# Optimization experiments

Measured on AMD Instinct MI355X. Metric: run time of the kernel, lower is better.

## Reference

```python
import jax, jax.numpy as jnp
import numpy as np

B, S, D, H = 2, 2048, 1024, 16
HD = D // H  # head dim = 64


def setup_inputs() -> dict:
    key = jax.random.key(0)
    ks = jax.random.split(key, 9)
    std = 0.02
    return {
        "hidden_states": jax.random.normal(ks[0], (B, S, D), jnp.float32),
        "wq": jax.random.normal(ks[1], (D, D), jnp.float32) * std,
        "bq": jnp.zeros((D,), jnp.float32),
        "wk": jax.random.normal(ks[2], (D, D), jnp.float32) * std,
        "bk": jnp.zeros((D,), jnp.float32),
        "wv": jax.random.normal(ks[3], (D, D), jnp.float32) * std,
        "bv": jnp.zeros((D,), jnp.float32),
        "wo": jax.random.normal(ks[4], (D, D), jnp.float32) * std,
        "bo": jnp.zeros((D,), jnp.float32),
    }


def reference(hidden_states, wq, bq, wk, bk, wv, bv, wo, bo):
    b, s, d = hidden_states.shape
    # projections (torch Linear: x @ W.T + b; here weights stored as [in,out]-equivalent transpose)
    q = hidden_states @ wq.T + bq
    k = hidden_states @ wk.T + bk
    v = hidden_states @ wv.T + bv
    # [b, h, s, hd]
    q = q.reshape(b, s, H, HD).transpose(0, 2, 1, 3)
    k = k.reshape(b, s, H, HD).transpose(0, 2, 1, 3)
    v = v.reshape(b, s, H, HD).transpose(0, 2, 1, 3)
    scores = jnp.einsum("bhqd,bhkd->bhqk", q, k) / jnp.sqrt(jnp.float32(HD))
    probs = jax.nn.softmax(scores, axis=-1)  # dropout p=0 (eval)
    ctx = jnp.einsum("bhqk,bhkd->bhqd", probs, v)
    ctx = ctx.transpose(0, 2, 1, 3).reshape(b, s, d)
    return ctx @ wo.T + bo
```

## Files before the change

kernel.cpp:

```cpp
#include <hip/hip_runtime.h>
#include <math.h>
#include <stdint.h>

constexpr int BB  = 2;
constexpr int SS  = 2048;
constexpr int DD  = 1024;
constexpr int HH  = 16;
constexpr int HDD = 64;
constexpr int MM  = BB * SS;

typedef uint16_t u16;
typedef __attribute__((ext_vector_type(4))) float    f32x4;
typedef __attribute__((ext_vector_type(8))) _Float16 f16x8;
typedef __attribute__((ext_vector_type(4))) _Float16 f16x4;
typedef __attribute__((ext_vector_type(8))) short    s16x8;
typedef __attribute__((ext_vector_type(4))) unsigned int u32x4;

__device__ __forceinline__ u16 to_f16(float f) {
    const _Float16 h = (_Float16)f;
    return __builtin_bit_cast(u16, h);
}

__device__ __forceinline__ f32x4 mfma32(s16x8 a, s16x8 b, f32x4 c) {
    return __builtin_amdgcn_mfma_f32_16x16x32_f16(
        __builtin_bit_cast(f16x8, a), __builtin_bit_cast(f16x8, b), c, 0, 0, 0);
}
__device__ __forceinline__ f32x4 mfma32_ff(s16x8 a, f16x8 b, f32x4 c) {
    return __builtin_amdgcn_mfma_f32_16x16x32_f16(
        __builtin_bit_cast(f16x8, a), b, c, 0, 0, 0);
}

__device__ __forceinline__ void load_lds16(const void* g, void* l) {
    __builtin_amdgcn_global_load_lds(
        (const __attribute__((address_space(1))) void*)g,
        (__attribute__((address_space(3))) void*)l, 16, 0, 0);
}

__global__ __launch_bounds__(256) void cast_all(
    const float* __restrict__ x,
    const float* __restrict__ w0, const float* __restrict__ w1,
    const float* __restrict__ w2, const float* __restrict__ w3,
    u16* __restrict__ xb, u16* __restrict__ wb)
{
    const int blk = blockIdx.x, tid = threadIdx.x;
    const float* src; u16* dst; int idx;
    if (blk < 2048) { src = x; dst = xb; idx = blk * 256 + tid; }
    else {
        const int b2 = blk - 2048, which = b2 >> 9;
        src = (which == 0) ? w0 : (which == 1) ? w1 : (which == 2) ? w2 : w3;
        dst = wb + ((size_t)which << 20);
        idx = (b2 & 511) * 256 + tid;
    }
    const float4* in4 = (const float4*)src;
    const float4 a = in4[idx * 2], b = in4[idx * 2 + 1];
    s16x8 v;
    v[0] = (short)to_f16(a.x); v[1] = (short)to_f16(a.y);
    v[2] = (short)to_f16(a.z); v[3] = (short)to_f16(a.w);
    v[4] = (short)to_f16(b.x); v[5] = (short)to_f16(b.y);
    v[6] = (short)to_f16(b.z); v[7] = (short)to_f16(b.w);
    *(s16x8*)(dst + (size_t)idx * 8) = v;
}

template <bool SWAP>
__device__ __forceinline__ void kloop(
    const u16* __restrict__ Ag, const u16* __restrict__ Wg,
    u16* Abase, u16* Bbase, const int K, const int KH,
    const int c0, const int c1,
    const int lane, const int wm, const int wn, f32x4 (&acc)[4][4])
{
    load_lds16(Ag + (size_t)c0 * 16 * K, Abase + c0 * 512);
    load_lds16(Ag + (size_t)c1 * 16 * K, Abase + c1 * 512);
    load_lds16(Wg + (size_t)c0 * 16 * K, Bbase + c0 * 512);
    load_lds16(Wg + (size_t)c1 * 16 * K, Bbase + c1 * 512);

    for (int k0 = 0; k0 < KH; k0 += 32) {
        const int buf = (k0 >> 5) & 1;
        __syncthreads();
        if (k0 + 32 < KH) {
            const int nb_ = (buf ^ 1) * 4096;
            load_lds16(Ag + (size_t)c0 * 16 * K + k0 + 32, Abase + nb_ + c0 * 512);
            load_lds16(Ag + (size_t)c1 * 16 * K + k0 + 32, Abase + nb_ + c1 * 512);
            load_lds16(Wg + (size_t)c0 * 16 * K + k0 + 32, Bbase + nb_ + c0 * 512);
            load_lds16(Wg + (size_t)c1 * 16 * K + k0 + 32, Bbase + nb_ + c1 * 512);
        }
        const u16* Acur = Abase + buf * 4096;
        const u16* Bcur = Bbase + buf * 4096;

        s16x8 af[4], bf4[4];
#pragma unroll
        for (int i = 0; i < 4; ++i) {
            const int row = wm + i * 16 + (lane & 15);
            const int u   = (lane >> 4) ^ (row & 3);
            af[i] = *(const s16x8*)(Acur + (size_t)row * 32 + u * 8);
        }
#pragma unroll
        for (int j = 0; j < 4; ++j) {
            const int row = wn + j * 16 + (lane & 15);
            const int u   = (lane >> 4) ^ (row & 3);
            bf4[j] = *(const s16x8*)(Bcur + (size_t)row * 32 + u * 8);
        }
#pragma unroll
        for (int i = 0; i < 4; ++i)
#pragma unroll
            for (int j = 0; j < 4; ++j)
                acc[i][j] = SWAP ? mfma32(bf4[j], af[i], acc[i][j])
                                 : mfma32(af[i], bf4[j], acc[i][j]);
    }
}

template <int MODE>
__global__ __launch_bounds__(512) void gemm_mfma(
    const u16* __restrict__ A, const u16* __restrict__ Wb,
    const float* __restrict__ b0, const float* __restrict__ b1,
    const float* __restrict__ b2,
    float* __restrict__ outf, u16* __restrict__ outq, u16* __restrict__ outv,
    const int K)
{
    __shared__ u16 smem[32768];
    u16* As = smem;
    u16* Bs = smem + 16384;

    const int tid = threadIdx.x, lane = tid & 63, wid = tid >> 6;
    const int grp = wid >> 2, w4 = wid & 3;
    const int quad = lane >> 4;
    const int bm = blockIdx.y * 128;
    const int nb = blockIdx.x * 128;
    const int which = nb >> 10;
    const int ncol  = nb & 1023;
    const int KH = K >> 1;
    const u16* Wblk = Wb + ((size_t)which << 20) + (size_t)ncol * K;

    const int srow = lane >> 2;
    const int lu   = (lane & 3) ^ (srow & 3);
    const u16* Ag = A    + (size_t)(bm + srow) * K + grp * KH + lu * 8;
    const u16* Wg = Wblk + (size_t)srow       * K + grp * KH + lu * 8;
    const int c0 = w4 * 2, c1 = c0 + 1;
    u16* Abase = As + grp * 8192;
    u16* Bbase = Bs + grp * 8192;

    f32x4 acc[4][4];
#pragma unroll
    for (int i = 0; i < 4; ++i)
#pragma unroll
        for (int j = 0; j < 4; ++j) { f32x4 z = {0.f, 0.f, 0.f, 0.f}; acc[i][j] = z; }

    const int wm = (w4 >> 1) * 64, wn = (w4 & 1) * 64;
    const bool swap = (MODE == 0) || (which < 2);
    if (swap) kloop<true>(Ag, Wg, Abase, Bbase, K, KH, c0, c1, lane, wm, wn, acc);
    else      kloop<false>(Ag, Wg, Abase, Bbase, K, KH, c0, c1, lane, wm, wn, acc);

    __syncthreads();
    float* rp = (float*)smem;
    const int slot = (w4 * 64 + lane) * 4;
    if (grp == 1) {
#pragma unroll
        for (int i = 0; i < 4; ++i)
#pragma unroll
            for (int j = 0; j < 4; ++j)
                *(f32x4*)(rp + (i * 4 + j) * 1024 + slot) = acc[i][j];
    }
    __syncthreads();
    if (grp != 0) return;
#pragma unroll
    for (int i = 0; i < 4; ++i)
#pragma unroll
        for (int j = 0; j < 4; ++j)
            acc[i][j] += *(const f32x4*)(rp + (i * 4 + j) * 1024 + slot);

    if (MODE == 0) {
#pragma unroll
        for (int j = 0; j < 4; ++j) {
            const int n0 = nb + wn + 16 * j + quad * 4;
            const float4 bv = *(const float4*)&b0[n0];
#pragma unroll
            for (int i = 0; i < 4; ++i) {
                const int m = bm + wm + 16 * i + (lane & 15);
                f32x4 w = acc[i][j];
                w[0] += bv.x; w[1] += bv.y; w[2] += bv.z; w[3] += bv.w;
                *(f32x4*)&outf[(size_t)m * 1024 + n0] = w;
            }
        }
    } else if (which < 2) {
        const float* bias = which ? b1 : b0;
        const float scale = which ? 1.0f : 0.125f;
        u16* outb = outq + ((size_t)which << 22);
        const int h = (ncol + wn) >> 6;
#pragma unroll
        for (int j = 0; j < 4; ++j) {
            const int nl0 = ncol + wn + 16 * j + quad * 4;
            const float4 bv = *(const float4*)&bias[nl0];
            const int hd0 = 16 * j + quad * 4;
#pragma unroll
            for (int i = 0; i < 4; ++i) {
                const int m = bm + wm + 16 * i + (lane & 15);
                const int b_ = m >> 11, s = m & 2047;
                f16x4 w;
                w[0] = (_Float16)((acc[i][j][0] + bv.x) * scale);
                w[1] = (_Float16)((acc[i][j][1] + bv.y) * scale);
                w[2] = (_Float16)((acc[i][j][2] + bv.z) * scale);
                w[3] = (_Float16)((acc[i][j][3] + bv.w) * scale);
                *(f16x4*)&outb[(((size_t)(b_ * HH + h)) * SS + s) * HDD + hd0] = w;
            }
        }
    } else {
        const int kt = ((bm + wm) & 2047) >> 6;
        const int b_ = (bm + wm) >> 11;
#pragma unroll
        for (int j = 0; j < 4; ++j) {
            const int nl = ncol + wn + 16 * j + (lane & 15);
            const float bb = b2[nl];
            const int h = nl >> 6, hd = nl & 63;
            u16* vrow = outv + (((size_t)(b_ * HH + h)) * HDD + hd) * SS + kt * 64;
#pragma unroll
            for (int i = 0; i < 4; ++i) {
                const int p0 = (i >> 1) * 32 + quad * 8 + (i & 1) * 4;
                f16x4 w;
                w[0] = (_Float16)(acc[i][j][0] + bb);
                w[1] = (_Float16)(acc[i][j][1] + bb);
                w[2] = (_Float16)(acc[i][j][2] + bb);
                w[3] = (_Float16)(acc[i][j][3] + bb);
                *(f16x4*)&vrow[p0] = w;
            }
        }
    }
}

__global__ __launch_bounds__(512, 4) void attn_mfma(
    const u16* __restrict__ Q, const u16* __restrict__ Kg,
    const u16* __restrict__ Vt, u16* __restrict__ ctx)
{
    __shared__ u16 smem[32768];

    const int tid = threadIdx.x, lane = tid & 63, wid = tid >> 6;
    const int grp = wid >> 2, w4 = wid & 3;
    const int quad = lane >> 4;
    const int bh = blockIdx.y, q0 = blockIdx.x * 128;
    const u16* Qb = Q  + (size_t)bh * SS * HDD;
    const u16* Kb = Kg + (size_t)bh * SS * HDD + (size_t)grp * 1024 * HDD;
    const u16* Vb = Vt + (size_t)bh * HDD * SS + grp * 1024;

    u16* Kbase = smem + grp * 8192;
    u16* Vbase = smem + 16384 + grp * 8192;

    const int qa = q0 + w4 * 32 + (lane & 15);
    const s16x8 bq0a = *(const s16x8*)(Qb + (size_t)qa * HDD + quad * 8);
    const s16x8 bq1a = *(const s16x8*)(Qb + (size_t)qa * HDD + 32 + quad * 8);
    const s16x8 bq0b = *(const s16x8*)(Qb + (size_t)(qa + 16) * HDD + quad * 8);
    const s16x8 bq1b = *(const s16x8*)(Qb + (size_t)(qa + 16) * HDD + 32 + quad * 8);

    f32x4 oa[4], ob[4];
    f32x4 la4 = {0.f, 0.f, 0.f, 0.f}, lb4 = {0.f, 0.f, 0.f, 0.f};
#pragma unroll
    for (int m = 0; m < 4; ++m) {
        f32x4 z = {0.f, 0.f, 0.f, 0.f};
        oa[m] = z; ob[m] = z;
    }
    const s16x8 ones = {15360, 15360, 15360, 15360,
                        15360, 15360, 15360, 15360};

    const int c0 = w4 * 2, c1 = c0 + 1;
    const int r0 = (c0 * 64 + lane) >> 3, lu0 = ((lane & 7) ^ (r0 & 7));
    const int r1 = (c1 * 64 + lane) >> 3, lu1 = ((lane & 7) ^ (r1 & 7));
    const u16* Kp0 = Kb + (size_t)r0 * HDD + lu0 * 8;
    const u16* Kp1 = Kb + (size_t)r1 * HDD + lu1 * 8;
    const u16* Vp0 = Vb + (size_t)r0 * SS + lu0 * 8;
    const u16* Vp1 = Vb + (size_t)r1 * SS + lu1 * 8;

    load_lds16(Kp0, Kbase + c0 * 512);
    load_lds16(Kp1, Kbase + c1 * 512);
    load_lds16(Vp0, Vbase + c0 * 512);
    load_lds16(Vp1, Vbase + c1 * 512);

    for (int kt = 0; kt < 16; ++kt) {
        const int buf = kt & 1;
        __syncthreads();

        if (kt + 1 < 16) {
            const int nb_ = (buf ^ 1) * 4096;
            load_lds16(Kp0 + (size_t)(kt + 1) * 64 * HDD, Kbase + nb_ + c0 * 512);
            load_lds16(Kp1 + (size_t)(kt + 1) * 64 * HDD, Kbase + nb_ + c1 * 512);
            load_lds16(Vp0 + (kt + 1) * 64, Vbase + nb_ + c0 * 512);
            load_lds16(Vp1 + (kt + 1) * 64, Vbase + nb_ + c1 * 512);
        }
        const u16* Kbuf = Kbase + buf * 4096;
        const u16* Vbuf = Vbase + buf * 4096;

        f32x4 Sa[4], Sb[4];
#pragma unroll
        for (int j = 0; j < 4; ++j) {
            const int row = j * 16 + (lane & 15);
            const int sw = lane & 7;
            const s16x8 ak0 = *(const s16x8*)(Kbuf + (size_t)row * 64 + ((quad    ) ^ sw) * 8);
            const s16x8 ak1 = *(const s16x8*)(Kbuf + (size_t)row * 64 + ((quad + 4) ^ sw) * 8);
            f32x4 za = {0.f, 0.f, 0.f, 0.f};
            za = mfma32(ak0, bq0a, za);
            za = mfma32(ak1, bq1a, za);
            Sa[j] = za;
            f32x4 zb = {0.f, 0.f, 0.f, 0.f};
            zb = mfma32(ak0, bq0b, zb);
            zb = mfma32(ak1, bq1b, zb);
            Sb[j] = zb;
        }

        f16x8 pb0a, pb1a, pb0b, pb1b;
        {
            u32x4 u;
            u[0] = __builtin_bit_cast(unsigned int, __builtin_amdgcn_cvt_pkrtz(__expf(Sa[0][0]), __expf(Sa[0][1])));
            u[1] = __builtin_bit_cast(unsigned int, __builtin_amdgcn_cvt_pkrtz(__expf(Sa[0][2]), __expf(Sa[0][3])));
            u[2] = __builtin_bit_cast(unsigned int, __builtin_amdgcn_cvt_pkrtz(__expf(Sa[1][0]), __expf(Sa[1][1])));
            u[3] = __builtin_bit_cast(unsigned int, __builtin_amdgcn_cvt_pkrtz(__expf(Sa[1][2]), __expf(Sa[1][3])));
            pb0a = __builtin_bit_cast(f16x8, u);
            u[0] = __builtin_bit_cast(unsigned int, __builtin_amdgcn_cvt_pkrtz(__expf(Sa[2][0]), __expf(Sa[2][1])));
            u[1] = __builtin_bit_cast(unsigned int, __builtin_amdgcn_cvt_pkrtz(__expf(Sa[2][2]), __expf(Sa[2][3])));
            u[2] = __builtin_bit_cast(unsigned int, __builtin_amdgcn_cvt_pkrtz(__expf(Sa[3][0]), __expf(Sa[3][1])));
            u[3] = __builtin_bit_cast(unsigned int, __builtin_amdgcn_cvt_pkrtz(__expf(Sa[3][2]), __expf(Sa[3][3])));
            pb1a = __builtin_bit_cast(f16x8, u);
            u[0] = __builtin_bit_cast(unsigned int, __builtin_amdgcn_cvt_pkrtz(__expf(Sb[0][0]), __expf(Sb[0][1])));
            u[1] = __builtin_bit_cast(unsigned int, __builtin_amdgcn_cvt_pkrtz(__expf(Sb[0][2]), __expf(Sb[0][3])));
            u[2] = __builtin_bit_cast(unsigned int, __builtin_amdgcn_cvt_pkrtz(__expf(Sb[1][0]), __expf(Sb[1][1])));
            u[3] = __builtin_bit_cast(unsigned int, __builtin_amdgcn_cvt_pkrtz(__expf(Sb[1][2]), __expf(Sb[1][3])));
            pb0b = __builtin_bit_cast(f16x8, u);
            u[0] = __builtin_bit_cast(unsigned int, __builtin_amdgcn_cvt_pkrtz(__expf(Sb[2][0]), __expf(Sb[2][1])));
            u[1] = __builtin_bit_cast(unsigned int, __builtin_amdgcn_cvt_pkrtz(__expf(Sb[2][2]), __expf(Sb[2][3])));
            u[2] = __builtin_bit_cast(unsigned int, __builtin_amdgcn_cvt_pkrtz(__expf(Sb[3][0]), __expf(Sb[3][1])));
            u[3] = __builtin_bit_cast(unsigned int, __builtin_amdgcn_cvt_pkrtz(__expf(Sb[3][2]), __expf(Sb[3][3])));
            pb1b = __builtin_bit_cast(f16x8, u);
        }

        la4 = mfma32_ff(ones, pb0a, la4);
        la4 = mfma32_ff(ones, pb1a, la4);
        lb4 = mfma32_ff(ones, pb0b, lb4);
        lb4 = mfma32_ff(ones, pb1b, lb4);

#pragma unroll
        for (int m = 0; m < 4; ++m) {
            const int row = m * 16 + (lane & 15);
            const int sw = lane & 7;
            const s16x8 v0 = *(const s16x8*)(Vbuf + (size_t)row * 64 + ((quad    ) ^ sw) * 8);
            const s16x8 v1 = *(const s16x8*)(Vbuf + (size_t)row * 64 + ((quad + 4) ^ sw) * 8);
            oa[m] = mfma32_ff(v0, pb0a, oa[m]);
            oa[m] = mfma32_ff(v1, pb1a, oa[m]);
            ob[m] = mfma32_ff(v0, pb0b, ob[m]);
            ob[m] = mfma32_ff(v1, pb1b, ob[m]);
        }
    }

    __syncthreads();
    float* ep = (float*)smem;
    float* lp = ep + 8 * 1088;
    if (grp == 1) {
#pragma unroll
        for (int sub = 0; sub < 2; ++sub) {
            const float* src = (sub == 0) ? (const float*)&oa[0] : (const float*)&ob[0];
            float* base = ep + (w4 * 2 + sub) * 1088 + (lane & 15) * 68 + quad * 4;
#pragma unroll
            for (int m = 0; m < 4; ++m)
                *(f32x4*)(base + m * 16) = *(const f32x4*)(src + m * 4);
        }
        if (quad == 0) {
            lp[(w4 * 2 + 0) * 16 + (lane & 15)] = la4[0];
            lp[(w4 * 2 + 1) * 16 + (lane & 15)] = lb4[0];
        }
    }
    __syncthreads();
    if (grp == 0) {
        const int b_ = bh >> 4, h = bh & 15;
#pragma unroll
        for (int sub = 0; sub < 2; ++sub) {
            const f32x4* own = (sub == 0) ? &oa[0] : &ob[0];
            const float lown = (sub == 0) ? la4[0] : lb4[0];
            const float inv = 1.f / (lown + lp[(w4 * 2 + sub) * 16 + (lane & 15)]);
            const float* base = ep + (w4 * 2 + sub) * 1088 + (lane & 15) * 68 + quad * 4;
            const int s_idx = q0 + w4 * 32 + sub * 16 + (lane & 15);
            u16* orow = ctx + ((size_t)(b_ * SS + s_idx)) * DD + h * HDD;
#pragma unroll
            for (int m = 0; m < 4; ++m) {
                const f32x4 part = *(const f32x4*)(base + m * 16);
                f16x4 w;
#pragma unroll
                for (int r = 0; r < 4; ++r)
                    w[r] = (_Float16)((own[m][r] + part[r]) * inv);
                *(f16x4*)(orow + m * 16 + quad * 4) = w;
            }
        }
    }
}

extern "C" void kernel_launch(void* const* d_in, const int* in_sizes, int n_in,
                              void* d_out, int out_size, void* d_ws, size_t ws_size,
                              hipStream_t stream)
{
    const float* x  = (const float*)d_in[0];
    const float* wq = (const float*)d_in[1];
    const float* bq = (const float*)d_in[2];
    const float* wk = (const float*)d_in[3];
    const float* bk = (const float*)d_in[4];
    const float* wv = (const float*)d_in[5];
    const float* bv = (const float*)d_in[6];
    const float* wo = (const float*)d_in[7];
    const float* bo = (const float*)d_in[8];

    u16* xb   = (u16*)d_ws;
    u16* wb   = xb  + ((size_t)4  << 20);
    u16* qk   = wb  + ((size_t)4  << 20);
    u16* vtw  = qk  + ((size_t)8  << 20);
    u16* ctxb = vtw + ((size_t)4  << 20);

    cast_all<<<4096, 256, 0, stream>>>(x, wq, wk, wv, wo, xb, wb);

    gemm_mfma<1><<<dim3(24, 32), 512, 0, stream>>>(
        xb, wb, bq, bk, bv, nullptr, qk, vtw, DD);

    attn_mfma<<<dim3(16, 32), 512, 0, stream>>>(
        qk, qk + ((size_t)4 << 20), vtw, ctxb);

    gemm_mfma<0><<<dim3(8, 32), 512, 0, stream>>>(
        ctxb, wb + ((size_t)3 << 20), bo, nullptr, nullptr,
        (float*)d_out, nullptr, nullptr, DD);
}
```

Baseline: 194.5 us.

## Split GEMM K dimension across four wave groups with tree reduction

Both GEMM kernels now launch 1024 threads per block instead of 512, and the K dimension is split four ways across wave groups instead of two. LDS doubles to 128 KB to hold the four per-group double buffers. The partial accumulators are combined in a two-level LDS reduction before the epilogue. The aim is more in-flight waves and shorter per-wave K loops to hide latency, at the cost of more LDS, lower block occupancy per CU, and extra reduction syncs and traffic.

```diff
diff --git a/kernel.cpp b/kernel.cpp
--- a/kernel.cpp
+++ b/kernel.cpp
@@ -64,7 +64,7 @@
 template <bool SWAP>
 __device__ __forceinline__ void kloop(
     const u16* __restrict__ Ag, const u16* __restrict__ Wg,
-    u16* Abase, u16* Bbase, const int K, const int KH,
+    u16* Abase, u16* Bbase, const int K, const int KQ,
     const int c0, const int c1,
     const int lane, const int wm, const int wn, f32x4 (&acc)[4][4])
 {
@@ -73,10 +73,10 @@
     load_lds16(Wg + (size_t)c0 * 16 * K, Bbase + c0 * 512);
     load_lds16(Wg + (size_t)c1 * 16 * K, Bbase + c1 * 512);
 
-    for (int k0 = 0; k0 < KH; k0 += 32) {
+    for (int k0 = 0; k0 < KQ; k0 += 32) {
         const int buf = (k0 >> 5) & 1;
         __syncthreads();
-        if (k0 + 32 < KH) {
+        if (k0 + 32 < KQ) {
             const int nb_ = (buf ^ 1) * 4096;
             load_lds16(Ag + (size_t)c0 * 16 * K + k0 + 32, Abase + nb_ + c0 * 512);
             load_lds16(Ag + (size_t)c1 * 16 * K + k0 + 32, Abase + nb_ + c1 * 512);
@@ -109,16 +109,16 @@
 }
 
 template <int MODE>
-__global__ __launch_bounds__(512) void gemm_mfma(
+__global__ __launch_bounds__(1024) void gemm_mfma(
     const u16* __restrict__ A, const u16* __restrict__ Wb,
     const float* __restrict__ b0, const float* __restrict__ b1,
     const float* __restrict__ b2,
     float* __restrict__ outf, u16* __restrict__ outq, u16* __restrict__ outv,
     const int K)
 {
-    __shared__ u16 smem[32768];
+    __shared__ u16 smem[65536];
     u16* As = smem;
-    u16* Bs = smem + 16384;
+    u16* Bs = smem + 32768;
 
     const int tid = threadIdx.x, lane = tid & 63, wid = tid >> 6;
     const int grp = wid >> 2, w4 = wid & 3;
@@ -127,13 +127,13 @@
     const int nb = blockIdx.x * 128;
     const int which = nb >> 10;
     const int ncol  = nb & 1023;
-    const int KH = K >> 1;
+    const int KQ = K >> 2;
     const u16* Wblk = Wb + ((size_t)which << 20) + (size_t)ncol * K;
 
     const int srow = lane >> 2;
     const int lu   = (lane & 3) ^ (srow & 3);
-    const u16* Ag = A    + (size_t)(bm + srow) * K + grp * KH + lu * 8;
-    const u16* Wg = Wblk + (size_t)srow       * K + grp * KH + lu * 8;
+    const u16* Ag = A    + (size_t)(bm + srow) * K + grp * KQ + lu * 8;
+    const u16* Wg = Wblk + (size_t)srow       * K + grp * KQ + lu * 8;
     const int c0 = w4 * 2, c1 = c0 + 1;
     u16* Abase = As + grp * 8192;
     u16* Bbase = Bs + grp * 8192;
@@ -146,18 +146,36 @@
 
     const int wm = (w4 >> 1) * 64, wn = (w4 & 1) * 64;
     const bool swap = (MODE == 0) || (which < 2);
-    if (swap) kloop<true>(Ag, Wg, Abase, Bbase, K, KH, c0, c1, lane, wm, wn, acc);
-    else      kloop<false>(Ag, Wg, Abase, Bbase, K, KH, c0, c1, lane, wm, wn, acc);
-
-    __syncthreads();
+    if (swap) kloop<true>(Ag, Wg, Abase, Bbase, K, KQ, c0, c1, lane, wm, wn, acc);
+    else      kloop<false>(Ag, Wg, Abase, Bbase, K, KQ, c0, c1, lane, wm, wn, acc);
+
     float* rp = (float*)smem;
     const int slot = (w4 * 64 + lane) * 4;
-    if (grp == 1) {
+    __syncthreads();
+    if (grp == 1 || grp == 3) {
+        float* reg = rp + (grp >> 1) * 16384;
 #pragma unroll
         for (int i = 0; i < 4; ++i)
 #pragma unroll
             for (int j = 0; j < 4; ++j)
-                *(f32x4*)(rp + (i * 4 + j) * 1024 + slot) = acc[i][j];
+                *(f32x4*)(reg + (i * 4 + j) * 1024 + slot) = acc[i][j];
+    }
+    __syncthreads();
+    if (grp == 0) {
+#pragma unroll
+        for (int i = 0; i < 4; ++i)
+#pragma unroll
+            for (int j = 0; j < 4; ++j)
+                acc[i][j] += *(const f32x4*)(rp + (i * 4 + j) * 1024 + slot);
+    } else if (grp == 2) {
+        float* reg = rp + 16384;
+#pragma unroll
+        for (int i = 0; i < 4; ++i)
+#pragma unroll
+            for (int j = 0; j < 4; ++j) {
+                acc[i][j] += *(const f32x4*)(reg + (i * 4 + j) * 1024 + slot);
+                *(f32x4*)(reg + (i * 4 + j) * 1024 + slot) = acc[i][j];
+            }
     }
     __syncthreads();
     if (grp != 0) return;
@@ -165,7 +183,7 @@
     for (int i = 0; i < 4; ++i)
 #pragma unroll
         for (int j = 0; j < 4; ++j)
-            acc[i][j] += *(const f32x4*)(rp + (i * 4 + j) * 1024 + slot);
+            acc[i][j] += *(const f32x4*)(rp + 16384 + (i * 4 + j) * 1024 + slot);
 
     if (MODE == 0) {
 #pragma unroll
@@ -189,7 +207,7 @@
         for (int j = 0; j < 4; ++j) {
             const int nl0 = ncol + wn + 16 * j + quad * 4;
             const float4 bv = *(const float4*)&bias[nl0];
-            const int hd0 = 16 * j + quad * 4;
+            const int hd0 = (nl0 & 63);
 #pragma unroll
             for (int i = 0; i < 4; ++i) {
                 const int m = bm + wm + 16 * i + (lane & 15);
@@ -408,13 +426,13 @@
 
     cast_all<<<4096, 256, 0, stream>>>(x, wq, wk, wv, wo, xb, wb);
 
-    gemm_mfma<1><<<dim3(24, 32), 512, 0, stream>>>(
+    gemm_mfma<1><<<dim3(24, 32), 1024, 0, stream>>>(
         xb, wb, bq, bk, bv, nullptr, qk, vtw, DD);
 
     attn_mfma<<<dim3(16, 32), 512, 0, stream>>>(
         qk, qk + ((size_t)4 << 20), vtw, ctxb);
 
-    gemm_mfma<0><<<dim3(8, 32), 512, 0, stream>>>(
+    gemm_mfma<0><<<dim3(8, 32), 1024, 0, stream>>>(
         ctxb, wb + ((size_t)3 << 20), bo, nullptr, nullptr,
         (float*)d_out, nullptr, nullptr, DD);
 }
```

Result: no change. 194.9 us (+0.2%).
